# Kernel tuning notes

Hardware: AMD Instinct MI355X
Metric: run time of the kernel (lower is better)

The kernel has to match this reference:

```python
import jax, jax.numpy as jnp
import numpy as np

EPS = 1e-15
PROJ_EPS = 4e-3  # float32 eps used by PoincareBall.proj

def artanh(x):
    x = jnp.clip(x, -1.0 + EPS, 1.0 - EPS)
    return 0.5 * (jnp.log1p(x) - jnp.log1p(-x))

def poincare_proj(x, c):
    # clip points to stay strictly inside the ball of radius 1/sqrt(c)
    norm = jnp.maximum(jnp.linalg.norm(x, axis=-1, keepdims=True), EPS)
    maxnorm = (1.0 - PROJ_EPS) / jnp.sqrt(c)
    return jnp.where(norm > maxnorm, x / norm * maxnorm, x)

def mobius_add(x, y, c):
    # x, y broadcast to [..., dim]
    x2 = jnp.sum(x * x, axis=-1, keepdims=True)
    y2 = jnp.sum(y * y, axis=-1, keepdims=True)
    xy = jnp.sum(x * y, axis=-1, keepdims=True)
    num = (1.0 + 2.0 * c * xy + c * y2) * x + (1.0 - c * x2) * y
    denom = 1.0 + 2.0 * c * xy + (c ** 2) * x2 * y2
    return num / jnp.maximum(denom, EPS)

def poincare_sqdist(x, y, c):
    sqrt_c = jnp.sqrt(c)
    diff_norm = jnp.linalg.norm(mobius_add(-x, y, c), axis=-1)
    dist = 2.0 / sqrt_c * artanh(sqrt_c * diff_norm)
    return dist ** 2

def setup_inputs() -> dict:
    key = jax.random.key(0)
    k1, k2 = jax.random.split(key)
    N, K, D = 8192, 256, 128
    node_repr = jax.random.normal(k1, (N, D), dtype=jnp.float32) * 0.01  # points near origin of the ball
    centroid_weight = jax.random.normal(k2, (K, D), dtype=jnp.float32) * 0.01
    mask = jnp.ones((N, 1), dtype=jnp.float32)
    c = jnp.ones((1,), dtype=jnp.float32)
    return {"node_repr": node_repr, "mask": mask, "centroid_weight": centroid_weight, "c": c}

def reference(node_repr, mask, centroid_weight, c):
    cc = c[0]
    centroid_repr = poincare_proj(centroid_weight, cc)            # [K, D]
    # broadcasted pairwise hyperbolic squared distances: [N, K]
    node_centroid_dist = poincare_sqdist(node_repr[:, None, :], centroid_repr[None, :, :], cc)
    node_centroid_dist = node_centroid_dist[None]                  # [1, N, K]
    graph_centroid_dist = jnp.sum(node_centroid_dist, axis=1) / jnp.sum(mask)  # [1, K]
    return (graph_centroid_dist, node_centroid_dist)
```

## Files before the change

kernel.cpp:

```cpp
#include <hip/hip_runtime.h>
#include <hip/hip_bf16.h>
#include <math.h>

#define KTOT 256
#define TN 128
#define TK 64

typedef __attribute__((ext_vector_type(8))) short bf16x8;
typedef __attribute__((ext_vector_type(4))) float f32x4;

static __device__ inline bf16x8 pack8(float4 a, float4 b) {
    union { __hip_bfloat162 h[4]; bf16x8 v; } u;
    u.h[0] = __float22bfloat162_rn(make_float2(a.x, a.y));
    u.h[1] = __float22bfloat162_rn(make_float2(a.z, a.w));
    u.h[2] = __float22bfloat162_rn(make_float2(b.x, b.y));
    u.h[3] = __float22bfloat162_rn(make_float2(b.z, b.w));
    return u.v;
}

__global__ __launch_bounds__(256) void scd_fused(
    const float* __restrict__ node,
    const float* __restrict__ maskp,
    const float* __restrict__ cw,
    const float* __restrict__ cptr,
    float* __restrict__ out,
    unsigned* __restrict__ cnt,
    float* __restrict__ part,
    int nbn, int nblk, int maskN)
{
    __shared__ short xs[TN][128];
    __shared__ short ys[TK][128];
    __shared__ float x2_s[TN];
    __shared__ float y2r_s[TK], scale_s[TK], y2p_s[TK];
    __shared__ float part_s[4][TK];
    __shared__ int lastblk;

    const int tid = threadIdx.x;
    const int w = tid >> 6;
    const int l = tid & 63;
    const int bn = blockIdx.x >> 2;
    const int kq = blockIdx.x & 3;
    const int nb = bn * TN;
    const int kb = kq * TK;
    const float c = cptr[0];

    const float4* nf4 = (const float4*)(node + (size_t)nb * 128);
    #pragma unroll
    for (int i = 0; i < 8; ++i) {
        int e = tid + 256 * i;
        int r = e >> 4, j = e & 15;
        float4 a = nf4[r * 32 + j * 2];
        float4 b = nf4[r * 32 + j * 2 + 1];
        float p = a.x * a.x + a.y * a.y + a.z * a.z + a.w * a.w
                + b.x * b.x + b.y * b.y + b.z * b.z + b.w * b.w;
        p += __shfl_xor(p, 1);
        p += __shfl_xor(p, 2);
        p += __shfl_xor(p, 4);
        p += __shfl_xor(p, 8);
        if ((tid & 15) == 0) x2_s[r] = p;
        *(bf16x8*)&xs[r][8 * (j ^ (r & 15))] = pack8(a, b);
    }
    const float4* yf4 = (const float4*)(cw + (size_t)kb * 128);
    #pragma unroll
    for (int i = 0; i < 4; ++i) {
        int e = tid + 256 * i;
        int r = e >> 4, j = e & 15;
        float4 a = yf4[r * 32 + j * 2];
        float4 b = yf4[r * 32 + j * 2 + 1];
        float p = a.x * a.x + a.y * a.y + a.z * a.z + a.w * a.w
                + b.x * b.x + b.y * b.y + b.z * b.z + b.w * b.w;
        p += __shfl_xor(p, 1);
        p += __shfl_xor(p, 2);
        p += __shfl_xor(p, 4);
        p += __shfl_xor(p, 8);
        if ((tid & 15) == 0) y2r_s[r] = p;
        *(bf16x8*)&ys[r][8 * (j ^ (r & 15))] = pack8(a, b);
    }
    __syncthreads();

    if (tid < TK) {
        float ss = y2r_s[tid];
        float norm = fmaxf(sqrtf(ss), 1e-15f);
        float maxn = (1.0f - 4e-3f) / sqrtf(c);
        float sc = (norm > maxn) ? (maxn / norm) : 1.0f;
        scale_s[tid] = sc;
        y2p_s[tid] = ss * sc * sc;
    }
    __syncthreads();

    const int q = l >> 4;
    const int rA0 = 32 * w + (l & 15);
    const int rA1 = rA0 + 16;
    const int key = l & 15;

    f32x4 acc[2][4];
    #pragma unroll
    for (int sb = 0; sb < 2; ++sb)
        #pragma unroll
        for (int ct = 0; ct < 4; ++ct) acc[sb][ct] = (f32x4){0.f, 0.f, 0.f, 0.f};

    #pragma unroll
    for (int ks = 0; ks < 4; ++ks) {
        int jl = q + 4 * ks;
        bf16x8 A0 = *(bf16x8*)&xs[rA0][8 * (jl ^ key)];
        bf16x8 A1 = *(bf16x8*)&xs[rA1][8 * (jl ^ key)];
        #pragma unroll
        for (int ct = 0; ct < 4; ++ct) {
            bf16x8 B = *(bf16x8*)&ys[16 * ct + (l & 15)][8 * (jl ^ key)];
            acc[0][ct] = __builtin_amdgcn_mfma_f32_16x16x32_bf16(A0, B, acc[0][ct], 0, 0, 0);
            acc[1][ct] = __builtin_amdgcn_mfma_f32_16x16x32_bf16(A1, B, acc[1][ct], 0, 0, 0);
        }
    }

    const float sqrt_c = sqrtf(c);
    const float dscale = (2.0f / sqrt_c) * 0.34657359028f;
    const float twoc = 2.0f * c;
    const float cc2 = c * c;

    float scv[4], y2v[4], abase[4], ccy2[4];
    #pragma unroll
    for (int ct = 0; ct < 4; ++ct) {
        int kk = 16 * ct + (l & 15);
        scv[ct] = scale_s[kk];
        y2v[ct] = y2p_s[kk];
        abase[ct] = 1.0f + c * y2v[ct];
        ccy2[ct] = cc2 * y2v[ct];
    }

    float kpart[4] = {0.f, 0.f, 0.f, 0.f};
    #pragma unroll
    for (int sb = 0; sb < 2; ++sb) {
        #pragma unroll
        for (int reg = 0; reg < 4; ++reg) {
            int rloc = 32 * w + 16 * sb + 4 * q + reg;
            float x2 = x2_s[rloc];
            float b = 1.0f - c * x2;
            float* po = out + KTOT + (size_t)(nb + rloc) * KTOT + kb + (l & 15);
            #pragma unroll
            for (int ct = 0; ct < 4; ++ct) {
                float xy = -acc[sb][ct][reg] * scv[ct];
                float a = fmaf(twoc, xy, abase[ct]);
                float den = fmaf(twoc, xy, fmaf(ccy2[ct], x2, 1.0f));
                float num2 = fmaf(a * a, x2, fmaf(b * b, y2v[ct], 2.0f * a * b * xy));
                num2 = fmaxf(num2, 0.0f);
                den = fmaxf(den, 1e-15f);
                float z = sqrt_c * __builtin_amdgcn_sqrtf(num2) * __builtin_amdgcn_rcpf(den);
                z = fminf(fmaxf(z, 0.0f), 0.99999994f);
                float arg = (1.0f + z) * __builtin_amdgcn_rcpf(1.0f - z);
                float d = dscale * __builtin_amdgcn_logf(arg);
                float s = d * d;
                po[16 * ct] = s;
                kpart[ct] += s;
            }
        }
    }

    #pragma unroll
    for (int ct = 0; ct < 4; ++ct) {
        kpart[ct] += __shfl_xor(kpart[ct], 16);
        kpart[ct] += __shfl_xor(kpart[ct], 32);
    }
    if (l < 16) {
        #pragma unroll
        for (int ct = 0; ct < 4; ++ct) part_s[w][l + 16 * ct] = kpart[ct];
    }
    __syncthreads();
    if (tid < TK) {
        float v = part_s[0][tid] + part_s[1][tid] + part_s[2][tid] + part_s[3][tid];
        __hip_atomic_store(&part[(size_t)bn * KTOT + kb + tid], v,
                           __ATOMIC_RELAXED, __HIP_MEMORY_SCOPE_AGENT);
    }

    __syncthreads();
    if (tid == 0) {
        unsigned old = __hip_atomic_fetch_add(cnt, 1u, __ATOMIC_RELAXED, __HIP_MEMORY_SCOPE_AGENT);
        lastblk = ((old % (unsigned)nblk) == (unsigned)(nblk - 1));
    }
    __syncthreads();
    if (!lastblk) return;

    float p = 0.f;
    {
        const float4* m4 = (const float4*)maskp;
        int m4n = maskN >> 2;
        for (int i = tid; i < m4n; i += 256) {
            float4 v = m4[i];
            p += v.x + v.y + v.z + v.w;
        }
        p += __shfl_xor(p, 1);  p += __shfl_xor(p, 2);  p += __shfl_xor(p, 4);
        p += __shfl_xor(p, 8);  p += __shfl_xor(p, 16); p += __shfl_xor(p, 32);
    }
    __syncthreads();
    if (l == 0) part_s[0][w] = p;
    __syncthreads();
    float inv = 1.0f / (part_s[0][0] + part_s[0][1] + part_s[0][2] + part_s[0][3]);

    float s0 = 0.f, s1 = 0.f, s2 = 0.f, s3 = 0.f;
    const float* pc = part + tid;
    for (int b = 0; b + 3 < nbn; b += 4) {
        s0 += __hip_atomic_load(pc + (size_t)(b + 0) * KTOT, __ATOMIC_RELAXED, __HIP_MEMORY_SCOPE_AGENT);
        s1 += __hip_atomic_load(pc + (size_t)(b + 1) * KTOT, __ATOMIC_RELAXED, __HIP_MEMORY_SCOPE_AGENT);
        s2 += __hip_atomic_load(pc + (size_t)(b + 2) * KTOT, __ATOMIC_RELAXED, __HIP_MEMORY_SCOPE_AGENT);
        s3 += __hip_atomic_load(pc + (size_t)(b + 3) * KTOT, __ATOMIC_RELAXED, __HIP_MEMORY_SCOPE_AGENT);
    }
    out[tid] = ((s0 + s1) + (s2 + s3)) * inv;
}

extern "C" void kernel_launch(void* const* d_in, const int* in_sizes, int n_in,
                              void* d_out, int out_size, void* d_ws, size_t ws_size,
                              hipStream_t stream) {
    const float* node = (const float*)d_in[0];
    const float* mask = (const float*)d_in[1];
    const float* cw   = (const float*)d_in[2];
    const float* cp   = (const float*)d_in[3];
    float* out = (float*)d_out;
    unsigned* cnt = (unsigned*)d_ws;
    float* part = (float*)((char*)d_ws + 256);

    int N = in_sizes[0] / 128;
    int maskN = in_sizes[1];
    int nbn = N / TN;
    int nblk = nbn * (KTOT / TK);

    scd_fused<<<dim3(nblk), 256, 0, stream>>>(node, mask, cw, cp, out, cnt, part,
                                              nbn, nblk, maskN);
}
```

Before: 19.73 us.

## Load MFMA operands directly from global memory, dropping LDS staging

Removes the shared-memory staging of node and centroid tiles. Each lane now loads its MFMA fragments straight from global memory, converts them to bf16 in registers, and accumulates the squared norms with shuffles. The mask sum is computed by every block up front instead of only by the last block. The partial-sum layout is transposed so the final reduction reads contiguous rows, and that loop is hardcoded to 64 partials. This removes LDS traffic and two block barriers, at the cost of redundant global reads of centroid rows across waves, uncoalesced 32-byte loads, and extra mask reads in every block.

```diff
diff --git a/kernel.cpp b/kernel.cpp
--- a/kernel.cpp
+++ b/kernel.cpp
@@ -9,13 +9,16 @@
 typedef __attribute__((ext_vector_type(8))) short bf16x8;
 typedef __attribute__((ext_vector_type(4))) float f32x4;
 
-static __device__ inline bf16x8 pack8(float4 a, float4 b) {
+static __device__ __forceinline__ bf16x8 pack8(float4 a, float4 b) {
     union { __hip_bfloat162 h[4]; bf16x8 v; } u;
     u.h[0] = __float22bfloat162_rn(make_float2(a.x, a.y));
     u.h[1] = __float22bfloat162_rn(make_float2(a.z, a.w));
     u.h[2] = __float22bfloat162_rn(make_float2(b.x, b.y));
     u.h[3] = __float22bfloat162_rn(make_float2(b.z, b.w));
     return u.v;
+}
+static __device__ __forceinline__ float sq4(float4 v) {
+    return fmaf(v.x, v.x, fmaf(v.y, v.y, fmaf(v.z, v.z, v.w * v.w)));
 }
 
 __global__ __launch_bounds__(256) void scd_fused(
@@ -28,102 +31,87 @@
     float* __restrict__ part,
     int nbn, int nblk, int maskN)
 {
-    __shared__ short xs[TN][128];
-    __shared__ short ys[TK][128];
-    __shared__ float x2_s[TN];
-    __shared__ float y2r_s[TK], scale_s[TK], y2p_s[TK];
     __shared__ float part_s[4][TK];
+    __shared__ float wred[4];
     __shared__ int lastblk;
 
     const int tid = threadIdx.x;
-    const int w = tid >> 6;
-    const int l = tid & 63;
-    const int bn = blockIdx.x >> 2;
-    const int kq = blockIdx.x & 3;
-    const int nb = bn * TN;
-    const int kb = kq * TK;
+    const int w = tid >> 6, l = tid & 63;
+    const int q = l >> 4, r15 = l & 15;
+    const int bn = blockIdx.x >> 2, kq = blockIdx.x & 3;
+    const int nb = bn * TN, kb = kq * TK;
     const float c = cptr[0];
 
-    const float4* nf4 = (const float4*)(node + (size_t)nb * 128);
-    #pragma unroll
-    for (int i = 0; i < 8; ++i) {
-        int e = tid + 256 * i;
-        int r = e >> 4, j = e & 15;
-        float4 a = nf4[r * 32 + j * 2];
-        float4 b = nf4[r * 32 + j * 2 + 1];
-        float p = a.x * a.x + a.y * a.y + a.z * a.z + a.w * a.w
-                + b.x * b.x + b.y * b.y + b.z * b.z + b.w * b.w;
-        p += __shfl_xor(p, 1);
-        p += __shfl_xor(p, 2);
-        p += __shfl_xor(p, 4);
-        p += __shfl_xor(p, 8);
-        if ((tid & 15) == 0) x2_s[r] = p;
-        *(bf16x8*)&xs[r][8 * (j ^ (r & 15))] = pack8(a, b);
-    }
-    const float4* yf4 = (const float4*)(cw + (size_t)kb * 128);
-    #pragma unroll
-    for (int i = 0; i < 4; ++i) {
-        int e = tid + 256 * i;
-        int r = e >> 4, j = e & 15;
-        float4 a = yf4[r * 32 + j * 2];
-        float4 b = yf4[r * 32 + j * 2 + 1];
-        float p = a.x * a.x + a.y * a.y + a.z * a.z + a.w * a.w
-                + b.x * b.x + b.y * b.y + b.z * b.z + b.w * b.w;
-        p += __shfl_xor(p, 1);
-        p += __shfl_xor(p, 2);
-        p += __shfl_xor(p, 4);
-        p += __shfl_xor(p, 8);
-        if ((tid & 15) == 0) y2r_s[r] = p;
-        *(bf16x8*)&ys[r][8 * (j ^ (r & 15))] = pack8(a, b);
-    }
-    __syncthreads();
-
-    if (tid < TK) {
-        float ss = y2r_s[tid];
-        float norm = fmaxf(sqrtf(ss), 1e-15f);
-        float maxn = (1.0f - 4e-3f) / sqrtf(c);
-        float sc = (norm > maxn) ? (maxn / norm) : 1.0f;
-        scale_s[tid] = sc;
-        y2p_s[tid] = ss * sc * sc;
-    }
-    __syncthreads();
-
-    const int q = l >> 4;
-    const int rA0 = 32 * w + (l & 15);
-    const int rA1 = rA0 + 16;
-    const int key = l & 15;
+    float mp = 0.f;
+    {
+        const float4* m4 = (const float4*)maskp;
+        int m4n = maskN >> 2;
+        for (int e = tid; e < m4n; e += 256) {
+            float4 v = m4[e];
+            mp += (v.x + v.y) + (v.z + v.w);
+        }
+    }
+
+    const float4* nf4 = (const float4*)node;
+    const float4* cf4 = (const float4*)cw;
+    const int rowA0 = nb + 32 * w + r15;
 
     f32x4 acc[2][4];
     #pragma unroll
     for (int sb = 0; sb < 2; ++sb)
         #pragma unroll
         for (int ct = 0; ct < 4; ++ct) acc[sb][ct] = (f32x4){0.f, 0.f, 0.f, 0.f};
+    float x2a[2] = {0.f, 0.f};
+    float y2a[4] = {0.f, 0.f, 0.f, 0.f};
 
     #pragma unroll
     for (int ks = 0; ks < 4; ++ks) {
-        int jl = q + 4 * ks;
-        bf16x8 A0 = *(bf16x8*)&xs[rA0][8 * (jl ^ key)];
-        bf16x8 A1 = *(bf16x8*)&xs[rA1][8 * (jl ^ key)];
+        const int ko = 8 * ks + 2 * q;
+        float4 a00 = nf4[(size_t)rowA0 * 32 + ko];
+        float4 a01 = nf4[(size_t)rowA0 * 32 + ko + 1];
+        float4 a10 = nf4[(size_t)(rowA0 + 16) * 32 + ko];
+        float4 a11 = nf4[(size_t)(rowA0 + 16) * 32 + ko + 1];
+        x2a[0] += sq4(a00) + sq4(a01);
+        x2a[1] += sq4(a10) + sq4(a11);
+        bf16x8 A0 = pack8(a00, a01);
+        bf16x8 A1 = pack8(a10, a11);
         #pragma unroll
         for (int ct = 0; ct < 4; ++ct) {
-            bf16x8 B = *(bf16x8*)&ys[16 * ct + (l & 15)][8 * (jl ^ key)];
+            size_t rb = (size_t)(kb + 16 * ct + r15) * 32 + ko;
+            float4 b0 = cf4[rb];
+            float4 b1 = cf4[rb + 1];
+            y2a[ct] += sq4(b0) + sq4(b1);
+            bf16x8 B = pack8(b0, b1);
             acc[0][ct] = __builtin_amdgcn_mfma_f32_16x16x32_bf16(A0, B, acc[0][ct], 0, 0, 0);
             acc[1][ct] = __builtin_amdgcn_mfma_f32_16x16x32_bf16(A1, B, acc[1][ct], 0, 0, 0);
         }
     }
 
+    #pragma unroll
+    for (int sb = 0; sb < 2; ++sb) {
+        x2a[sb] += __shfl_xor(x2a[sb], 16);
+        x2a[sb] += __shfl_xor(x2a[sb], 32);
+    }
+    #pragma unroll
+    for (int ct = 0; ct < 4; ++ct) {
+        y2a[ct] += __shfl_xor(y2a[ct], 16);
+        y2a[ct] += __shfl_xor(y2a[ct], 32);
+    }
+
     const float sqrt_c = sqrtf(c);
-    const float dscale = (2.0f / sqrt_c) * 0.34657359028f;
+    const float maxn = (1.0f - 4e-3f) * __builtin_amdgcn_rcpf(sqrt_c);
+    const float dscale = (2.0f * 0.34657359028f) * __builtin_amdgcn_rcpf(sqrt_c);
     const float twoc = 2.0f * c;
     const float cc2 = c * c;
 
     float scv[4], y2v[4], abase[4], ccy2[4];
     #pragma unroll
     for (int ct = 0; ct < 4; ++ct) {
-        int kk = 16 * ct + (l & 15);
-        scv[ct] = scale_s[kk];
-        y2v[ct] = y2p_s[kk];
-        abase[ct] = 1.0f + c * y2v[ct];
+        float nrm = fmaxf(sqrtf(y2a[ct]), 1e-15f);
+        float sc = (nrm > maxn) ? maxn * __builtin_amdgcn_rcpf(nrm) : 1.0f;
+        scv[ct] = sc;
+        y2v[ct] = y2a[ct] * sc * sc;
+        abase[ct] = fmaf(c, y2v[ct], 1.0f);
         ccy2[ct] = cc2 * y2v[ct];
     }
 
@@ -132,10 +120,10 @@
     for (int sb = 0; sb < 2; ++sb) {
         #pragma unroll
         for (int reg = 0; reg < 4; ++reg) {
-            int rloc = 32 * w + 16 * sb + 4 * q + reg;
-            float x2 = x2_s[rloc];
-            float b = 1.0f - c * x2;
-            float* po = out + KTOT + (size_t)(nb + rloc) * KTOT + kb + (l & 15);
+            const int rl = 4 * q + reg;
+            const float x2 = __shfl(x2a[sb], rl);
+            const float b = fmaf(-c, x2, 1.0f);
+            float* po = out + KTOT + (size_t)(nb + 32 * w + 16 * sb + rl) * KTOT + kb + r15;
             #pragma unroll
             for (int ct = 0; ct < 4; ++ct) {
                 float xy = -acc[sb][ct][reg] * scv[ct];
@@ -160,14 +148,17 @@
         kpart[ct] += __shfl_xor(kpart[ct], 16);
         kpart[ct] += __shfl_xor(kpart[ct], 32);
     }
+    mp += __shfl_xor(mp, 1);  mp += __shfl_xor(mp, 2);  mp += __shfl_xor(mp, 4);
+    mp += __shfl_xor(mp, 8);  mp += __shfl_xor(mp, 16); mp += __shfl_xor(mp, 32);
+    if (l == 0) wred[w] = mp;
     if (l < 16) {
         #pragma unroll
-        for (int ct = 0; ct < 4; ++ct) part_s[w][l + 16 * ct] = kpart[ct];
+        for (int ct = 0; ct < 4; ++ct) part_s[w][16 * ct + l] = kpart[ct];
     }
     __syncthreads();
     if (tid < TK) {
-        float v = part_s[0][tid] + part_s[1][tid] + part_s[2][tid] + part_s[3][tid];
-        __hip_atomic_store(&part[(size_t)bn * KTOT + kb + tid], v,
+        float v = (part_s[0][tid] + part_s[1][tid]) + (part_s[2][tid] + part_s[3][tid]);
+        __hip_atomic_store(&part[(size_t)(kb + tid) * nbn + bn], v,
                            __ATOMIC_RELAXED, __HIP_MEMORY_SCOPE_AGENT);
     }
 
@@ -179,31 +170,22 @@
     __syncthreads();
     if (!lastblk) return;
 
-    float p = 0.f;
-    {
-        const float4* m4 = (const float4*)maskp;
-        int m4n = maskN >> 2;
-        for (int i = tid; i < m4n; i += 256) {
-            float4 v = m4[i];
-            p += v.x + v.y + v.z + v.w;
-        }
-        p += __shfl_xor(p, 1);  p += __shfl_xor(p, 2);  p += __shfl_xor(p, 4);
-        p += __shfl_xor(p, 8);  p += __shfl_xor(p, 16); p += __shfl_xor(p, 32);
-    }
-    __syncthreads();
-    if (l == 0) part_s[0][w] = p;
-    __syncthreads();
-    float inv = 1.0f / (part_s[0][0] + part_s[0][1] + part_s[0][2] + part_s[0][3]);
-
-    float s0 = 0.f, s1 = 0.f, s2 = 0.f, s3 = 0.f;
-    const float* pc = part + tid;
-    for (int b = 0; b + 3 < nbn; b += 4) {
-        s0 += __hip_atomic_load(pc + (size_t)(b + 0) * KTOT, __ATOMIC_RELAXED, __HIP_MEMORY_SCOPE_AGENT);
-        s1 += __hip_atomic_load(pc + (size_t)(b + 1) * KTOT, __ATOMIC_RELAXED, __HIP_MEMORY_SCOPE_AGENT);
-        s2 += __hip_atomic_load(pc + (size_t)(b + 2) * KTOT, __ATOMIC_RELAXED, __HIP_MEMORY_SCOPE_AGENT);
-        s3 += __hip_atomic_load(pc + (size_t)(b + 3) * KTOT, __ATOMIC_RELAXED, __HIP_MEMORY_SCOPE_AGENT);
-    }
-    out[tid] = ((s0 + s1) + (s2 + s3)) * inv;
+    float msum = (wred[0] + wred[1]) + (wred[2] + wred[3]);
+    float inv = 1.0f / msum;
+
+    const float* pc = part + (size_t)tid * nbn;
+    float s[16];
+    #pragma unroll
+    for (int u = 0; u < 16; ++u)
+        s[u] = __hip_atomic_load(pc + u, __ATOMIC_RELAXED, __HIP_MEMORY_SCOPE_AGENT);
+    #pragma unroll
+    for (int g = 16; g < 64; g += 16)
+        #pragma unroll
+        for (int u = 0; u < 16; ++u)
+            s[u] += __hip_atomic_load(pc + g + u, __ATOMIC_RELAXED, __HIP_MEMORY_SCOPE_AGENT);
+    float t0 = ((s[0] + s[1]) + (s[2] + s[3])) + ((s[4] + s[5]) + (s[6] + s[7]));
+    float t1 = ((s[8] + s[9]) + (s[10] + s[11])) + ((s[12] + s[13]) + (s[14] + s[15]));
+    out[tid] = (t0 + t1) * inv;
 }
 
 extern "C" void kernel_launch(void* const* d_in, const int* in_sizes, int n_in,
```

New measurement: 26.08 us. +32.2%, slower.
